# Kernel tuning notes

Measured on AMD Instinct MI355X. Metric: run time of the kernel, lower is better.

Reference implementation:

```python
import jax, jax.numpy as jnp
import numpy as np
from jax import lax

BN_EPS = 1e-5
BNS = 1.0 / np.sqrt(1.0 + BN_EPS)  # eval-mode BatchNorm with mean=0, var=1, gamma=1, beta=0


def setup_inputs() -> dict:
    key = jax.random.key(0)
    ks = jax.random.split(key, 12)
    B, Cin, H, W = 8, 256, 128, 128
    NC, HD, RC, NL = 12, 64, 128, 3
    f = lambda k, shp, s: jax.random.normal(k, shp, jnp.float32) * s
    return dict(
        features=f(ks[0], (B, Cin, H, W), 1.0),
        segmentation=jax.random.uniform(ks[1], (B, NC, H, W), dtype=jnp.float32),
        W_rpn=f(ks[2], (RC, Cin, 3, 3), 0.02), b_rpn=jnp.zeros((RC,), jnp.float32),
        W_node=f(ks[3], (HD, RC), 0.08), b_node=jnp.zeros((HD,), jnp.float32),
        W_e1=f(ks[4], (2 * HD, HD), 0.08), b_e1=jnp.zeros((HD,), jnp.float32),
        W_e2=f(ks[5], (HD, HD), 0.1), b_e2=jnp.zeros((HD,), jnp.float32),
        W_g=f(ks[6], (NL, HD, HD), 0.1), b_g=jnp.zeros((NL, HD), jnp.float32),
        ln_g=jnp.ones((NL, HD), jnp.float32), ln_b=jnp.zeros((NL, HD), jnp.float32),
        glob_emb=f(ks[7], (NC, HD), 0.02),
        W_sp=f(ks[8], (HD, RC), 0.1), b_sp=jnp.zeros((RC,), jnp.float32),
    )


def _forward(features, segmentation, W_rpn, b_rpn, W_node, b_node, W_e1, b_e1,
             W_e2, b_e2, W_g, b_g, ln_g, ln_b, glob_emb, W_sp, b_sp):
    B, NC, H, W = segmentation.shape
    HD = W_node.shape[0]
    NL = W_g.shape[0]

    # ---- RegionProposalNetwork: 3x3 conv + BN(eval) + ReLU ----
    refined = lax.conv_general_dilated(
        features, W_rpn, (1, 1), 'SAME',
        dimension_numbers=('NCHW', 'OIHW', 'NCHW'))
    refined = jax.nn.relu((refined + b_rpn[None, :, None, None]) * BNS)  # [B,RC,H,W]

    # per-class 3x3 maxpool on segmentation, threshold -> binary masks
    pooled = lax.reduce_window(segmentation, -jnp.inf, lax.max,
                               (1, 1, 3, 3), (1, 1, 1, 1), 'SAME')
    masks = (pooled > 0.5).astype(features.dtype)  # [B,NC,H,W]

    # ---- NodeFeatureExtractor (1x1 conv is linear: conv(f*m)=(Wf)*m + b) ----
    yw = jnp.einsum('dk,bkhw->bdhw', W_node, refined)            # [B,HD,H,W]
    z = jax.nn.relu((yw + b_node[None, :, None, None]) * BNS)    # value inside mask region
    masked_sum = jnp.einsum('bdhw,bchw->bcd', z, masks)          # [B,NC,HD]
    mask_sum = masks.sum((2, 3))                                 # [B,NC]
    node_feats = masked_sum / (mask_sum[..., None] + 1e-6)       # [B,NC,HD]

    # ---- EdgeFeatureExtractor: all (i,j), i!=j, gated by class presence ----
    pairs = np.array([(i, j) for i in range(NC) for j in range(NC) if i != j])
    src = jnp.asarray(pairs[:, 0])  # [E]
    dst = jnp.asarray(pairs[:, 1])
    present = (mask_sum > 0).astype(features.dtype)              # [B,NC]
    valid = present[:, src] * present[:, dst]                    # [B,E]
    cat = jnp.concatenate([node_feats[:, src], node_feats[:, dst]], axis=-1)  # [B,E,2HD]
    h = jax.nn.relu(cat @ W_e1 + b_e1)
    edge_attr = (h @ W_e2 + b_e2) * valid[..., None]             # [B,E,HD]

    # ---- TissueGraphNetwork ----
    presence = (node_feats.sum(-1) != 0).astype(features.dtype)[..., None]  # [B,NC,1]
    seg_sum = jax.vmap(lambda m: jax.ops.segment_sum(m, dst, num_segments=NC))
    x = node_feats
    for l in range(NL):
        xw = x @ W_g[l]                                          # [B,NC,HD]
        msgs = xw[:, src] * edge_attr                            # [B,E,HD]
        agg = seg_sum(msgs) + b_g[l]
        xr = jax.nn.relu(agg)
        mu = xr.mean(-1, keepdims=True)
        var = ((xr - mu) ** 2).mean(-1, keepdims=True)
        normed = (xr - mu) / jnp.sqrt(var + 1e-5) * ln_g[l] + ln_b[l]
        x = normed + x if l > 0 else normed
    x = x * presence + glob_emb[None] * (1.0 - presence)         # [B,NC,HD]

    # ---- SpatialProjector ----
    spatial = jnp.einsum('bcd,bchw->bdhw', x, masks)             # [B,HD,H,W]
    out = jnp.einsum('do,bdhw->bohw', W_sp, spatial)             # [B,RC,H,W]
    out = jax.nn.relu((out + b_sp[None, :, None, None]) * BNS)
    return out


def reference(features, segmentation, W_rpn, b_rpn, W_node, b_node, W_e1, b_e1,
              W_e2, b_e2, W_g, b_g, ln_g, ln_b, glob_emb, W_sp, b_sp):
    return _forward(features, segmentation, W_rpn, b_rpn, W_node, b_node,
                    W_e1, b_e1, W_e2, b_e2, W_g, b_g, ln_g, ln_b,
                    glob_emb, W_sp, b_sp)
```

## Files before the change

### kernel.cpp

```cpp
#include <hip/hip_runtime.h>
#include <math.h>

#define BNS_F 0.9999950000374998f

typedef short short8 __attribute__((ext_vector_type(8)));
typedef float f32x4 __attribute__((ext_vector_type(4)));
typedef __attribute__((address_space(3))) void lds_void;
typedef const __attribute__((address_space(1))) void glb_void;

__device__ __forceinline__ unsigned short f2bf(float f) {
    unsigned u = __builtin_bit_cast(unsigned, f);
    unsigned r = (u + 0x7fffu + ((u >> 16) & 1u)) >> 16;
    return (unsigned short)r;
}
__device__ __forceinline__ float bf2f(unsigned short h) {
    unsigned u = ((unsigned)h) << 16;
    return __builtin_bit_cast(float, u);
}

__global__ __launch_bounds__(256) void convert_feat(
    const float* __restrict__ feat, unsigned short* __restrict__ Fbt)
{
    __shared__ unsigned short sb[64 * 270];
    int b = blockIdx.x >> 8;
    int px0 = (blockIdx.x & 255) * 64;
    int t = threadIdx.x, l = t & 63, w = t >> 6;

    for (int r = 0; r < 64; ++r) {
        int ic = r * 4 + w;
        float v = feat[((size_t)(b * 256 + ic)) * 16384 + px0 + l];
        sb[l * 270 + ic] = f2bf(v);
    }
    __syncthreads();

    uint4* dst = (uint4*)(Fbt + ((size_t)(b * 16384 + px0)) * 256);
    #pragma unroll
    for (int k = 0; k < 8; ++k) {
        int idx = k * 256 + t;
        int px = idx >> 5, piece = idx & 31;
        dst[idx] = *(const uint4*)(sb + px * 270 + piece * 8);
    }
}

__global__ __launch_bounds__(256) void reorg_w(
    const float* __restrict__ Wrpn, unsigned short* __restrict__ Wr)
{
    int oc = blockIdx.x;
    int ic = threadIdx.x;
    const float* src = Wrpn + ((size_t)oc * 256 + ic) * 9;
    #pragma unroll
    for (int tap = 0; tap < 9; ++tap)
        Wr[((size_t)tap * 128 + oc) * 256 + ic] = f2bf(src[tap]);
}

__global__ __launch_bounds__(128) void masks_kernel(
    const float* __restrict__ seg, float* __restrict__ masks,
    float* __restrict__ mask_sum)
{
    int bid = blockIdx.x;
    int h = bid & 127;
    int c = (bid >> 7) % 12;
    int b = bid / (128 * 12);
    int px = threadIdx.x;

    const float* s = seg + ((size_t)(b * 12 + c) * 128) * 128;
    float m = -INFINITY;
    #pragma unroll
    for (int dy = -1; dy <= 1; ++dy) {
        int y = h + dy;
        if (y < 0 || y > 127) continue;
        #pragma unroll
        for (int dx = -1; dx <= 1; ++dx) {
            int x = px + dx;
            if (x < 0 || x > 127) continue;
            m = fmaxf(m, s[y * 128 + x]);
        }
    }
    float v = (m > 0.5f) ? 1.0f : 0.0f;
    masks[((size_t)(b * 12 + c) * 128 + h) * 128 + px] = v;

    float cnt = v;
    #pragma unroll
    for (int off = 1; off < 64; off <<= 1) cnt += __shfl_xor(cnt, off, 64);
    if ((threadIdx.x & 63) == 0) atomicAdd(&mask_sum[b * 12 + c], cnt);
}

#define SWZ(col) (((col) >> 1) & 3)
#define BUF_BYTES 24960

__global__ __launch_bounds__(512) void conv_node_kernel(
    const unsigned short* __restrict__ Fbt, const unsigned short* __restrict__ Wr,
    const float* __restrict__ brpn, const float* __restrict__ Wnode,
    const float* __restrict__ bnode, const float* __restrict__ masks,
    const float* __restrict__ zero16, float* __restrict__ ms_rep)
{
    __shared__ __align__(16) unsigned char lds[49920];

    int wg = blockIdx.x;
    int bid = (wg & 7) * 128 + (wg >> 3);
    int h = bid & 127, b = bid >> 7;

    int t = threadIdx.x;
    int lane = t & 63;
    int wv = __builtin_amdgcn_readfirstlane(t >> 6);
    int mg = wv >> 1;
    int ng = wv & 1;
    int kg = lane >> 4;
    int ln15 = lane & 15;

    f32x4 acc[2][4];
    #pragma unroll
    for (int i = 0; i < 2; ++i)
        #pragma unroll
        for (int j = 0; j < 4; ++j) acc[i][j] = (f32x4){0.f, 0.f, 0.f, 0.f};

    const size_t fb_base = (size_t)b * 16384 * 256;

    auto stage = [&](int bsel, int ic0) {
        for (int c0 = 0; c0 < 1560; c0 += 512) {
            int c = c0 + t;
            unsigned ldsoff = (unsigned)bsel * BUF_BYTES + (unsigned)(c0 + wv * 64) * 16;
            if (c < 1560) {
                int sp = c & 3, cr = c >> 2;
                int col = cr % 130, row = cr / 130;
                int sl = (sp - SWZ(col)) & 3;
                int y = h - 1 + row;
                int x = col - 1;
                const void* gsrc = ((unsigned)y < 128u && (unsigned)x < 128u)
                    ? (const void*)(Fbt + fb_base + (size_t)(y * 128 + x) * 256
                                    + ic0 + sl * 8)
                    : (const void*)zero16;
                __builtin_amdgcn_global_load_lds(
                    (glb_void*)gsrc, (lds_void*)(lds + ldsoff), 16, 0, 0);
            }
        }
    };

    stage(0, 0);
    __syncthreads();

    for (int s = 0; s < 8; ++s) {
        int ic0 = s * 32;
        const unsigned char* buf = lds + (s & 1) * BUF_BYTES;

        #pragma unroll
        for (int dy = 0; dy < 3; ++dy) {
            #pragma unroll
            for (int dxi = 0; dxi < 3; ++dxi) {
                int tap = dy * 3 + dxi;
                const unsigned short* wp =
                    Wr + ((size_t)(tap * 128 + mg * 32 + ln15) * 256 + ic0 + kg * 8);
                short8 a0 = *(const short8*)wp;
                short8 a1 = *(const short8*)(wp + (size_t)16 * 256);
                short8 bf[4];
                #pragma unroll
                for (int nt = 0; nt < 4; ++nt) {
                    int col = ng * 64 + nt * 16 + ln15 + dxi;
                    unsigned off =
                        (unsigned)((dy * 130 + col) * 4 + ((kg + SWZ(col)) & 3)) * 16;
                    bf[nt] = *(const short8*)(buf + off);
                }
                #pragma unroll
                for (int nt = 0; nt < 4; ++nt) {
                    acc[0][nt] = __builtin_amdgcn_mfma_f32_16x16x32_bf16(
                        a0, bf[nt], acc[0][nt], 0, 0, 0);
                    acc[1][nt] = __builtin_amdgcn_mfma_f32_16x16x32_bf16(
                        a1, bf[nt], acc[1][nt], 0, 0, 0);
                }
            }
        }

        if (s < 7) stage((s + 1) & 1, ic0 + 32);
        __syncthreads();
    }

    unsigned short* refined = (unsigned short*)lds;
    #pragma unroll
    for (int mt = 0; mt < 2; ++mt) {
        #pragma unroll
        for (int nt = 0; nt < 4; ++nt) {
            int px = ng * 64 + nt * 16 + ln15;
            #pragma unroll
            for (int r = 0; r < 4; ++r) {
                int oc = mg * 32 + mt * 16 + kg * 4 + r;
                float v = fmaxf((acc[mt][nt][r] + brpn[oc]) * BNS_F, 0.f);
                refined[oc * 130 + px] = f2bf(v);
            }
        }
    }
    __syncthreads();

    float z0[8], z1[8];
    #pragma unroll
    for (int j = 0; j < 8; ++j) { z0[j] = 0.f; z1[j] = 0.f; }
    const float* wn = Wnode + (size_t)wv * 8 * 128;
    for (int k = 0; k < 128; ++k) {
        float r0 = bf2f(refined[k * 130 + lane]);
        float r1 = bf2f(refined[k * 130 + 64 + lane]);
        #pragma unroll
        for (int j = 0; j < 8; ++j) {
            float w = wn[j * 128 + k];
            z0[j] = fmaf(w, r0, z0[j]);
            z1[j] = fmaf(w, r1, z1[j]);
        }
    }
    #pragma unroll
    for (int j = 0; j < 8; ++j) {
        float bb = bnode[wv * 8 + j];
        z0[j] = fmaxf((z0[j] + bb) * BNS_F, 0.f);
        z1[j] = fmaxf((z1[j] + bb) * BNS_F, 0.f);
    }

    int rep = bid & 7;
    const float* mrow = masks + ((size_t)b * 12 * 128 + h) * 128;
    float* msb = ms_rep + ((size_t)(rep * 8 + b) * 12) * 64 + wv * 8;
    for (int c = 0; c < 12; ++c) {
        float m0 = mrow[(size_t)c * 16384 + lane];
        float m1 = mrow[(size_t)c * 16384 + 64 + lane];
        #pragma unroll
        for (int j = 0; j < 8; ++j) {
            float v = fmaf(z0[j], m0, z1[j] * m1);
            #pragma unroll
            for (int off2 = 1; off2 < 64; off2 <<= 1) v += __shfl_xor(v, off2, 64);
            if (lane == 0) atomicAdd(&msb[c * 64 + j], v);
        }
    }
}

__global__ __launch_bounds__(256) void edge_kernel(
    const float* __restrict__ ms_rep, const float* __restrict__ mask_sum,
    const float* __restrict__ We1, const float* __restrict__ be1,
    const float* __restrict__ We2, const float* __restrict__ be2,
    float* __restrict__ ea_g)
{
    int gb = blockIdx.x;
    int b = gb / 33, eg = gb % 33;
    int wv = threadIdx.x >> 6, d = threadIdx.x & 63;
    int e = eg * 4 + wv;
    int src = e / 11, jj = e % 11;
    int dst = jj + (jj >= src ? 1 : 0);

    float mssrc = 0.f, msdst = 0.f;
    #pragma unroll
    for (int rep = 0; rep < 8; ++rep) {
        mssrc += ms_rep[((size_t)(rep * 8 + b) * 12 + src) * 64 + d];
        msdst += ms_rep[((size_t)(rep * 8 + b) * 12 + dst) * 64 + d];
    }
    float cs = mask_sum[b * 12 + src], cd = mask_sum[b * 12 + dst];
    float nsrc = mssrc / (cs + 1e-6f);
    float ndst = msdst / (cd + 1e-6f);

    float hv = be1[d];
    for (int k = 0; k < 64; ++k) hv = fmaf(__shfl(nsrc, k, 64), We1[k * 64 + d], hv);
    for (int k = 0; k < 64; ++k) hv = fmaf(__shfl(ndst, k, 64), We1[(64 + k) * 64 + d], hv);
    hv = fmaxf(hv, 0.f);
    float av = be2[d];
    for (int k = 0; k < 64; ++k) av = fmaf(__shfl(hv, k, 64), We2[k * 64 + d], av);

    float valid = ((cs > 0.f) ? 1.f : 0.f) * ((cd > 0.f) ? 1.f : 0.f);
    ea_g[((size_t)b * 132 + e) * 64 + d] = av * valid;
}

__global__ __launch_bounds__(256) void graph_kernel(
    const float* __restrict__ ms_rep, const float* __restrict__ mask_sum,
    const float* __restrict__ ea_g,
    const float* __restrict__ Wg, const float* __restrict__ bg,
    const float* __restrict__ lng, const float* __restrict__ lnb,
    const float* __restrict__ glob, const float* __restrict__ Wsp,
    float* __restrict__ xs_out)
{
    __shared__ float nf[12 * 64];
    __shared__ float x [12 * 64];
    __shared__ float xw[12 * 64];
    __shared__ float ea[132 * 64];
    __shared__ float presence[12];

    int b = blockIdx.x;
    int t = threadIdx.x;

    for (int i = t; i < 768; i += 256) {
        int c = i >> 6, d = i & 63;
        float ms = 0.f;
        #pragma unroll
        for (int rep = 0; rep < 8; ++rep)
            ms += ms_rep[((size_t)(rep * 8 + b) * 12 + c) * 64 + d];
        nf[i] = ms / (mask_sum[b * 12 + c] + 1e-6f);
    }
    for (int i = t; i < 132 * 64; i += 256) ea[i] = ea_g[(size_t)b * 8448 + i];
    __syncthreads();

    for (int i = t; i < 768; i += 256) {
        int c = i >> 6;
        float v = nf[i];
        #pragma unroll
        for (int off = 1; off < 64; off <<= 1) v += __shfl_xor(v, off, 64);
        if ((i & 63) == 0) presence[c] = (v != 0.f) ? 1.f : 0.f;
        x[i] = nf[i];
    }
    __syncthreads();

    for (int l = 0; l < 3; ++l) {
        const float* wg = Wg + l * 4096;
        for (int i = t; i < 768; i += 256) {
            int c = i >> 6, d = i & 63;
            float v = 0.f;
            for (int k = 0; k < 64; ++k) v = fmaf(x[c * 64 + k], wg[k * 64 + d], v);
            xw[i] = v;
        }
        __syncthreads();
        for (int i = t; i < 768; i += 256) {
            int j = i >> 6, d = i & 63;
            float agg = bg[l * 64 + d];
            #pragma unroll
            for (int src2 = 0; src2 < 12; ++src2) {
                if (src2 == j) continue;
                int jj2 = j - (j > src2 ? 1 : 0);
                int e = src2 * 11 + jj2;
                agg = fmaf(xw[src2 * 64 + d], ea[e * 64 + d], agg);
            }
            float xr = fmaxf(agg, 0.f);
            float s = xr;
            #pragma unroll
            for (int off = 1; off < 64; off <<= 1) s += __shfl_xor(s, off, 64);
            float mu = s * (1.f / 64.f);
            float df = xr - mu;
            float s2 = df * df;
            #pragma unroll
            for (int off = 1; off < 64; off <<= 1) s2 += __shfl_xor(s2, off, 64);
            float var = s2 * (1.f / 64.f);
            float normed = df * (1.0f / sqrtf(var + 1e-5f)) * lng[l * 64 + d]
                           + lnb[l * 64 + d];
            nf[i] = (l > 0) ? (normed + x[i]) : normed;
        }
        __syncthreads();
        for (int i = t; i < 768; i += 256) x[i] = nf[i];
        __syncthreads();
    }

    for (int i = t; i < 768; i += 256) {
        int c = i >> 6;
        float p = presence[c];
        x[i] = x[i] * p + glob[c * 64 + (i & 63)] * (1.f - p);
    }
    __syncthreads();

    for (int i = t; i < 12 * 128; i += 256) {
        int c = i >> 7, o = i & 127;
        float v = 0.f;
        for (int k = 0; k < 64; ++k) v = fmaf(x[c * 64 + k], Wsp[k * 128 + o], v);
        xs_out[b * 1536 + i] = v;
    }
}

__global__ __launch_bounds__(256) void out_kernel(
    const float* __restrict__ xs, const float* __restrict__ masks,
    const float* __restrict__ bsp, float* __restrict__ out)
{
    __shared__ float xsl[12 * 128];
    __shared__ float ml[12 * 128];
    int bid = blockIdx.x;
    int h = bid & 127;
    int b = bid >> 7;
    int t = threadIdx.x;

    for (int i = t; i < 1536; i += 256) xsl[i] = xs[b * 1536 + i];
    for (int i = t; i < 1536; i += 256) {
        int c = i >> 7, px = i & 127;
        ml[i] = masks[((size_t)(b * 12 + c) * 128 + h) * 128 + px];
    }
    __syncthreads();

    int px = t & 127;
    int og = t >> 7;
    float m[12];
    #pragma unroll
    for (int c = 0; c < 12; ++c) m[c] = ml[c * 128 + px];

    float* ob = out + ((size_t)b * 128 * 128 + h) * 128 + px;
    for (int i = 0; i < 64; ++i) {
        int o = og * 64 + i;
        float s = 0.f;
        #pragma unroll
        for (int c = 0; c < 12; ++c) s = fmaf(xsl[c * 128 + o], m[c], s);
        ob[(size_t)o * 16384] = fmaxf((s + bsp[o]) * BNS_F, 0.f);
    }
}

extern "C" void kernel_launch(void* const* d_in, const int* in_sizes, int n_in,
                              void* d_out, int out_size, void* d_ws, size_t ws_size,
                              hipStream_t stream)
{
    const float* feat  = (const float*)d_in[0];
    const float* seg   = (const float*)d_in[1];
    const float* Wrpn  = (const float*)d_in[2];
    const float* brpn  = (const float*)d_in[3];
    const float* Wnode = (const float*)d_in[4];
    const float* bnode = (const float*)d_in[5];
    const float* We1   = (const float*)d_in[6];
    const float* be1   = (const float*)d_in[7];
    const float* We2   = (const float*)d_in[8];
    const float* be2   = (const float*)d_in[9];
    const float* Wg    = (const float*)d_in[10];
    const float* bg    = (const float*)d_in[11];
    const float* lng   = (const float*)d_in[12];
    const float* lnb   = (const float*)d_in[13];
    const float* glob  = (const float*)d_in[14];
    const float* Wsp   = (const float*)d_in[15];
    const float* bsp   = (const float*)d_in[16];
    float* out = (float*)d_out;

    unsigned short* Fbt = (unsigned short*)d_out;

    float* masks    = (float*)d_ws;
    float* ms_rep   = masks + 1572864;
    float* mask_sum = ms_rep + 49152;
    float* zero16   = mask_sum + 96;
    float* xs       = zero16 + 8;
    float* ea_g     = xs + 12288;
    unsigned short* Wr = (unsigned short*)(ea_g + 67584);

    hipMemsetAsync(ms_rep, 0, (49152 + 96 + 8) * sizeof(float), stream);

    convert_feat<<<2048, 256, 0, stream>>>(feat, Fbt);
    reorg_w<<<128, 256, 0, stream>>>(Wrpn, Wr);
    masks_kernel<<<8 * 12 * 128, 128, 0, stream>>>(seg, masks, mask_sum);
    conv_node_kernel<<<1024, 512, 0, stream>>>(Fbt, Wr, brpn, Wnode, bnode,
                                               masks, zero16, ms_rep);
    edge_kernel<<<264, 256, 0, stream>>>(ms_rep, mask_sum, We1, be1, We2, be2, ea_g);
    graph_kernel<<<8, 256, 0, stream>>>(ms_rep, mask_sum, ea_g,
                                        Wg, bg, lng, lnb, glob, Wsp, xs);
    out_kernel<<<1024, 256, 0, stream>>>(xs, masks, bsp, out);
}
```

Measured before the change: 455.9 us.

## Chunk-major bf16 feature layout with register-staged single-buffer conv loads

Changes the converted feature layout from pixel-major with 256 channels to chunks of 8 channels laid out over all pixels. This lets convert_feat run without an LDS transpose, using coalesced per-chunk stores. The conv kernel drops the async global_load_lds double buffer and instead prefetches the next channel slice into registers while computing, then writes it to a single LDS buffer after a barrier. LDS use shrinks, which may raise occupancy, at the cost of an extra barrier per stage and more register pressure. The new layout also spreads each pixel's channels across strided chunks, which may hurt the locality of the gathers.

New measurement: 465.8 us. 1.02x slower.

```diff
diff --git a/kernel.cpp b/kernel.cpp
--- a/kernel.cpp
+++ b/kernel.cpp
@@ -5,8 +5,6 @@
 
 typedef short short8 __attribute__((ext_vector_type(8)));
 typedef float f32x4 __attribute__((ext_vector_type(4)));
-typedef __attribute__((address_space(3))) void lds_void;
-typedef const __attribute__((address_space(1))) void glb_void;
 
 __device__ __forceinline__ unsigned short f2bf(float f) {
     unsigned u = __builtin_bit_cast(unsigned, f);
@@ -21,25 +19,22 @@
 __global__ __launch_bounds__(256) void convert_feat(
     const float* __restrict__ feat, unsigned short* __restrict__ Fbt)
 {
-    __shared__ unsigned short sb[64 * 270];
-    int b = blockIdx.x >> 8;
-    int px0 = (blockIdx.x & 255) * 64;
-    int t = threadIdx.x, l = t & 63, w = t >> 6;
-
-    for (int r = 0; r < 64; ++r) {
-        int ic = r * 4 + w;
-        float v = feat[((size_t)(b * 256 + ic)) * 16384 + px0 + l];
-        sb[l * 270 + ic] = f2bf(v);
-    }
-    __syncthreads();
-
-    uint4* dst = (uint4*)(Fbt + ((size_t)(b * 16384 + px0)) * 256);
-    #pragma unroll
-    for (int k = 0; k < 8; ++k) {
-        int idx = k * 256 + t;
-        int px = idx >> 5, piece = idx & 31;
-        dst[idx] = *(const uint4*)(sb + px * 270 + piece * 8);
-    }
+    int bid = blockIdx.x;
+    int pxc = bid & 63;
+    int icg = (bid >> 6) & 31;
+    int b   = bid >> 11;
+    int px  = pxc * 256 + threadIdx.x;
+
+    const float* src = feat + ((size_t)(b * 256 + icg * 8)) * 16384 + px;
+    unsigned v[4];
+    #pragma unroll
+    for (int i = 0; i < 4; ++i) {
+        unsigned lo = f2bf(src[(size_t)(2 * i)     * 16384]);
+        unsigned hi = f2bf(src[(size_t)(2 * i + 1) * 16384]);
+        v[i] = lo | (hi << 16);
+    }
+    uint4 o; o.x = v[0]; o.y = v[1]; o.z = v[2]; o.w = v[3];
+    *(uint4*)(Fbt + (((size_t)(b * 32 + icg) * 16384) + px) * 8) = o;
 }
 
 __global__ __launch_bounds__(256) void reorg_w(
@@ -86,7 +81,7 @@
 }
 
 #define SWZ(col) (((col) >> 1) & 3)
-#define BUF_BYTES 24960
+#define CHUNK_STRIDE (4 * 16384 * 8)
 
 __global__ __launch_bounds__(512) void conv_node_kernel(
     const unsigned short* __restrict__ Fbt, const unsigned short* __restrict__ Wr,
@@ -94,7 +89,7 @@
     const float* __restrict__ bnode, const float* __restrict__ masks,
     const float* __restrict__ zero16, float* __restrict__ ms_rep)
 {
-    __shared__ __align__(16) unsigned char lds[49920];
+    __shared__ __align__(16) unsigned char lds[33280];
 
     int wg = blockIdx.x;
     int bid = (wg & 7) * 128 + (wg >> 3);
@@ -114,34 +109,51 @@
         #pragma unroll
         for (int j = 0; j < 4; ++j) acc[i][j] = (f32x4){0.f, 0.f, 0.f, 0.f};
 
-    const size_t fb_base = (size_t)b * 16384 * 256;
-
-    auto stage = [&](int bsel, int ic0) {
-        for (int c0 = 0; c0 < 1560; c0 += 512) {
-            int c = c0 + t;
-            unsigned ldsoff = (unsigned)bsel * BUF_BYTES + (unsigned)(c0 + wv * 64) * 16;
-            if (c < 1560) {
-                int sp = c & 3, cr = c >> 2;
-                int col = cr % 130, row = cr / 130;
-                int sl = (sp - SWZ(col)) & 3;
-                int y = h - 1 + row;
-                int x = col - 1;
-                const void* gsrc = ((unsigned)y < 128u && (unsigned)x < 128u)
-                    ? (const void*)(Fbt + fb_base + (size_t)(y * 128 + x) * 256
-                                    + ic0 + sl * 8)
-                    : (const void*)zero16;
-                __builtin_amdgcn_global_load_lds(
-                    (glb_void*)gsrc, (lds_void*)(lds + ldsoff), 16, 0, 0);
-            }
-        }
-    };
-
-    stage(0, 0);
+    const unsigned short* p[4];
+    size_t inc[4];
+    unsigned woff[4];
+    bool act3 = (t < 24);
+    #pragma unroll
+    for (int r = 0; r < 4; ++r) {
+        int c = (r < 3) ? (r * 512 + t) : (1536 + t);
+        bool act = (r < 3) || act3;
+        int sp = c & 3, cr = c >> 2;
+        int col = cr % 130, row = cr / 130;
+        int sl = (sp - SWZ(col)) & 3;
+        int y = h - 1 + row;
+        int x = col - 1;
+        bool in = ((unsigned)y < 128u) && ((unsigned)x < 128u) && act;
+        p[r]   = in ? (Fbt + (((size_t)(b * 32 + sl) * 16384) + y * 128 + x) * 8)
+                    : (const unsigned short*)zero16;
+        inc[r] = in ? (size_t)CHUNK_STRIDE : 0;
+        woff[r] = (unsigned)c * 16;
+    }
+
+    {
+        uint4 s0 = *(const uint4*)p[0];
+        uint4 s1 = *(const uint4*)p[1];
+        uint4 s2 = *(const uint4*)p[2];
+        uint4 s3 = act3 ? *(const uint4*)p[3] : (uint4){0, 0, 0, 0};
+        p[0] += inc[0]; p[1] += inc[1]; p[2] += inc[2]; p[3] += inc[3];
+        *(uint4*)(lds + woff[0]) = s0;
+        *(uint4*)(lds + woff[1]) = s1;
+        *(uint4*)(lds + woff[2]) = s2;
+        if (act3) *(uint4*)(lds + woff[3]) = s3;
+    }
     __syncthreads();
 
     for (int s = 0; s < 8; ++s) {
         int ic0 = s * 32;
-        const unsigned char* buf = lds + (s & 1) * BUF_BYTES;
+
+        uint4 st0, st1, st2, st3;
+        bool pre = (s < 7);
+        if (pre) {
+            st0 = *(const uint4*)p[0];
+            st1 = *(const uint4*)p[1];
+            st2 = *(const uint4*)p[2];
+            st3 = act3 ? *(const uint4*)p[3] : (uint4){0, 0, 0, 0};
+            p[0] += inc[0]; p[1] += inc[1]; p[2] += inc[2]; p[3] += inc[3];
+        }
 
         #pragma unroll
         for (int dy = 0; dy < 3; ++dy) {
@@ -158,7 +170,7 @@
                     int col = ng * 64 + nt * 16 + ln15 + dxi;
                     unsigned off =
                         (unsigned)((dy * 130 + col) * 4 + ((kg + SWZ(col)) & 3)) * 16;
-                    bf[nt] = *(const short8*)(buf + off);
+                    bf[nt] = *(const short8*)(lds + off);
                 }
                 #pragma unroll
                 for (int nt = 0; nt < 4; ++nt) {
@@ -170,8 +182,14 @@
             }
         }
 
-        if (s < 7) stage((s + 1) & 1, ic0 + 32);
         __syncthreads();
+        if (pre) {
+            *(uint4*)(lds + woff[0]) = st0;
+            *(uint4*)(lds + woff[1]) = st1;
+            *(uint4*)(lds + woff[2]) = st2;
+            if (act3) *(uint4*)(lds + woff[3]) = st3;
+            __syncthreads();
+        }
     }
 
     unsigned short* refined = (unsigned short*)lds;
@@ -421,7 +439,7 @@
 
     hipMemsetAsync(ms_rep, 0, (49152 + 96 + 8) * sizeof(float), stream);
 
-    convert_feat<<<2048, 256, 0, stream>>>(feat, Fbt);
+    convert_feat<<<16384, 256, 0, stream>>>(feat, Fbt);
     reorg_w<<<128, 256, 0, stream>>>(Wrpn, Wr);
     masks_kernel<<<8 * 12 * 128, 128, 0, stream>>>(seg, masks, mask_sum);
     conv_node_kernel<<<1024, 512, 0, stream>>>(Fbt, Wr, brpn, Wnode, bnode,
```

## Chunk bf16 feature layout by 8 channels and fuse prep kernels

Applied to the files above, without the earlier changes.

Changes the bf16 feature buffer from pixel-major with 256 channels to chunks of 8 channels per pixel ([B,32,HW,8]). This lets the conversion kernel write without an LDS transpose and lets the conv staging use precomputed pointers that advance by a fixed stride. The feature conversion, weight reorganisation and mask kernels are merged into one launch. The conv kernel also gets a launch_bounds occupancy hint and interleaves its B-fragment loads with the MFMAs. Global reads during staging become more scattered across channel chunks, and the occupancy hint may constrain register allocation.

Result: slower. 492.5 us (+8.0%).

```diff
diff --git a/kernel.cpp b/kernel.cpp
--- a/kernel.cpp
+++ b/kernel.cpp
@@ -18,77 +18,71 @@
     return __builtin_bit_cast(float, u);
 }
 
-__global__ __launch_bounds__(256) void convert_feat(
-    const float* __restrict__ feat, unsigned short* __restrict__ Fbt)
-{
-    __shared__ unsigned short sb[64 * 270];
-    int b = blockIdx.x >> 8;
-    int px0 = (blockIdx.x & 255) * 64;
-    int t = threadIdx.x, l = t & 63, w = t >> 6;
-
-    for (int r = 0; r < 64; ++r) {
-        int ic = r * 4 + w;
-        float v = feat[((size_t)(b * 256 + ic)) * 16384 + px0 + l];
-        sb[l * 270 + ic] = f2bf(v);
-    }
-    __syncthreads();
-
-    uint4* dst = (uint4*)(Fbt + ((size_t)(b * 16384 + px0)) * 256);
-    #pragma unroll
-    for (int k = 0; k < 8; ++k) {
-        int idx = k * 256 + t;
-        int px = idx >> 5, piece = idx & 31;
-        dst[idx] = *(const uint4*)(sb + px * 270 + piece * 8);
-    }
-}
-
-__global__ __launch_bounds__(256) void reorg_w(
-    const float* __restrict__ Wrpn, unsigned short* __restrict__ Wr)
-{
-    int oc = blockIdx.x;
-    int ic = threadIdx.x;
-    const float* src = Wrpn + ((size_t)oc * 256 + ic) * 9;
-    #pragma unroll
-    for (int tap = 0; tap < 9; ++tap)
-        Wr[((size_t)tap * 128 + oc) * 256 + ic] = f2bf(src[tap]);
-}
-
-__global__ __launch_bounds__(128) void masks_kernel(
+__global__ __launch_bounds__(256) void prep_kernel(
+    const float* __restrict__ feat, unsigned short* __restrict__ Fbt,
+    const float* __restrict__ Wrpn, unsigned short* __restrict__ Wr,
     const float* __restrict__ seg, float* __restrict__ masks,
     float* __restrict__ mask_sum)
 {
     int bid = blockIdx.x;
-    int h = bid & 127;
-    int c = (bid >> 7) % 12;
-    int b = bid / (128 * 12);
-    int px = threadIdx.x;
-
-    const float* s = seg + ((size_t)(b * 12 + c) * 128) * 128;
-    float m = -INFINITY;
-    #pragma unroll
-    for (int dy = -1; dy <= 1; ++dy) {
-        int y = h + dy;
-        if (y < 0 || y > 127) continue;
-        #pragma unroll
-        for (int dx = -1; dx <= 1; ++dx) {
-            int x = px + dx;
-            if (x < 0 || x > 127) continue;
-            m = fmaxf(m, s[y * 128 + x]);
-        }
-    }
-    float v = (m > 0.5f) ? 1.0f : 0.0f;
-    masks[((size_t)(b * 12 + c) * 128 + h) * 128 + px] = v;
-
-    float cnt = v;
-    #pragma unroll
-    for (int off = 1; off < 64; off <<= 1) cnt += __shfl_xor(cnt, off, 64);
-    if ((threadIdx.x & 63) == 0) atomicAdd(&mask_sum[b * 12 + c], cnt);
+    int t = threadIdx.x;
+
+    if (bid < 16384) {
+        int pxc = bid & 63;
+        int icg = (bid >> 6) & 31;
+        int b   = bid >> 11;
+        int px  = pxc * 256 + t;
+        const float* src = feat + ((size_t)(b * 256 + icg * 8)) * 16384 + px;
+        unsigned v[4];
+        #pragma unroll
+        for (int i = 0; i < 4; ++i) {
+            unsigned lo = f2bf(src[(size_t)(2 * i)     * 16384]);
+            unsigned hi = f2bf(src[(size_t)(2 * i + 1) * 16384]);
+            v[i] = lo | (hi << 16);
+        }
+        uint4 o; o.x = v[0]; o.y = v[1]; o.z = v[2]; o.w = v[3];
+        *(uint4*)(Fbt + (((size_t)(b * 32 + icg) * 16384) + px) * 8) = o;
+    } else if (bid < 16512) {
+        int oc = bid - 16384;
+        const float* src = Wrpn + ((size_t)oc * 256 + t) * 9;
+        #pragma unroll
+        for (int tap = 0; tap < 9; ++tap)
+            Wr[((size_t)tap * 128 + oc) * 256 + t] = f2bf(src[tap]);
+    } else {
+        int mb = bid - 16512;
+        int h = (mb & 63) * 2 + (t >> 7);
+        int c = (mb >> 6) % 12;
+        int b = mb / (64 * 12);
+        int px = t & 127;
+
+        const float* s = seg + ((size_t)(b * 12 + c) * 128) * 128;
+        float m = -INFINITY;
+        #pragma unroll
+        for (int dy = -1; dy <= 1; ++dy) {
+            int y = h + dy;
+            if (y < 0 || y > 127) continue;
+            #pragma unroll
+            for (int dx = -1; dx <= 1; ++dx) {
+                int x = px + dx;
+                if (x < 0 || x > 127) continue;
+                m = fmaxf(m, s[y * 128 + x]);
+            }
+        }
+        float v = (m > 0.5f) ? 1.0f : 0.0f;
+        masks[((size_t)(b * 12 + c) * 128 + h) * 128 + px] = v;
+
+        float cnt = v;
+        #pragma unroll
+        for (int off = 1; off < 64; off <<= 1) cnt += __shfl_xor(cnt, off, 64);
+        if ((t & 63) == 0) atomicAdd(&mask_sum[b * 12 + c], cnt);
+    }
 }
 
 #define SWZ(col) (((col) >> 1) & 3)
 #define BUF_BYTES 24960
-
-__global__ __launch_bounds__(512) void conv_node_kernel(
+#define CHUNK_ELEMS (4u * 16384u * 8u)
+
+__global__ __launch_bounds__(512, 6) void conv_node_kernel(
     const unsigned short* __restrict__ Fbt, const unsigned short* __restrict__ Wr,
     const float* __restrict__ brpn, const float* __restrict__ Wnode,
     const float* __restrict__ bnode, const float* __restrict__ masks,
@@ -114,29 +108,40 @@
         #pragma unroll
         for (int j = 0; j < 4; ++j) acc[i][j] = (f32x4){0.f, 0.f, 0.f, 0.f};
 
-    const size_t fb_base = (size_t)b * 16384 * 256;
-
-    auto stage = [&](int bsel, int ic0) {
-        for (int c0 = 0; c0 < 1560; c0 += 512) {
-            int c = c0 + t;
-            unsigned ldsoff = (unsigned)bsel * BUF_BYTES + (unsigned)(c0 + wv * 64) * 16;
-            if (c < 1560) {
-                int sp = c & 3, cr = c >> 2;
-                int col = cr % 130, row = cr / 130;
-                int sl = (sp - SWZ(col)) & 3;
-                int y = h - 1 + row;
-                int x = col - 1;
-                const void* gsrc = ((unsigned)y < 128u && (unsigned)x < 128u)
-                    ? (const void*)(Fbt + fb_base + (size_t)(y * 128 + x) * 256
-                                    + ic0 + sl * 8)
-                    : (const void*)zero16;
-                __builtin_amdgcn_global_load_lds(
-                    (glb_void*)gsrc, (lds_void*)(lds + ldsoff), 16, 0, 0);
-            }
-        }
+    const unsigned short* zp = (const unsigned short*)zero16;
+
+    const unsigned short* pp[4];
+    #pragma unroll
+    for (int r = 0; r < 4; ++r) {
+        int c = (r < 3) ? (r * 512 + t) : (1536 + t);
+        bool act = (r < 3) || (t < 24);
+        int sp = c & 3, cr = c >> 2;
+        int col = cr % 130, row = cr / 130;
+        int sl = (sp - SWZ(col)) & 3;
+        int y = h - 1 + row, x = col - 1;
+        bool in = act && ((unsigned)y < 128u) && ((unsigned)x < 128u);
+        pp[r] = in ? (Fbt + (((size_t)(b * 32 + sl) * 16384) + y * 128 + x) * 8)
+                   : zp;
+    }
+
+    auto stage = [&](int bsel) {
+        #pragma unroll
+        for (int r = 0; r < 3; ++r) {
+            unsigned ldsoff = (unsigned)bsel * BUF_BYTES
+                            + (unsigned)(r * 512 + wv * 64) * 16;
+            __builtin_amdgcn_global_load_lds((glb_void*)pp[r],
+                (lds_void*)(lds + ldsoff), 16, 0, 0);
+            pp[r] += (pp[r] == zp) ? 0u : CHUNK_ELEMS;
+        }
+        if (t < 24) {
+            unsigned ldsoff = (unsigned)bsel * BUF_BYTES + 1536u * 16;
+            __builtin_amdgcn_global_load_lds((glb_void*)pp[3],
+                (lds_void*)(lds + ldsoff), 16, 0, 0);
+        }
+        pp[3] += (pp[3] == zp) ? 0u : CHUNK_ELEMS;
     };
 
-    stage(0, 0);
+    stage(0);
     __syncthreads();
 
     for (int s = 0; s < 8; ++s) {
@@ -152,25 +157,32 @@
                     Wr + ((size_t)(tap * 128 + mg * 32 + ln15) * 256 + ic0 + kg * 8);
                 short8 a0 = *(const short8*)wp;
                 short8 a1 = *(const short8*)(wp + (size_t)16 * 256);
-                short8 bf[4];
                 #pragma unroll
-                for (int nt = 0; nt < 4; ++nt) {
-                    int col = ng * 64 + nt * 16 + ln15 + dxi;
-                    unsigned off =
-                        (unsigned)((dy * 130 + col) * 4 + ((kg + SWZ(col)) & 3)) * 16;
-                    bf[nt] = *(const short8*)(buf + off);
-                }
-                #pragma unroll
-                for (int nt = 0; nt < 4; ++nt) {
-                    acc[0][nt] = __builtin_amdgcn_mfma_f32_16x16x32_bf16(
-                        a0, bf[nt], acc[0][nt], 0, 0, 0);
-                    acc[1][nt] = __builtin_amdgcn_mfma_f32_16x16x32_bf16(
-                        a1, bf[nt], acc[1][nt], 0, 0, 0);
+                for (int np = 0; np < 2; ++np) {
+                    short8 b0, b1;
+                    {
+                        int col0 = ng * 64 + (np * 2) * 16 + ln15 + dxi;
+                        unsigned off0 = (unsigned)((dy * 130 + col0) * 4
+                                        + ((kg + SWZ(col0)) & 3)) * 16;
+                        b0 = *(const short8*)(buf + off0);
+                        int col1 = col0 + 16;
+                        unsigned off1 = (unsigned)((dy * 130 + col1) * 4
+                                        + ((kg + SWZ(col1)) & 3)) * 16;
+                        b1 = *(const short8*)(buf + off1);
+                    }
+                    acc[0][np * 2]     = __builtin_amdgcn_mfma_f32_16x16x32_bf16(
+                        a0, b0, acc[0][np * 2], 0, 0, 0);
+                    acc[1][np * 2]     = __builtin_amdgcn_mfma_f32_16x16x32_bf16(
+                        a1, b0, acc[1][np * 2], 0, 0, 0);
+                    acc[0][np * 2 + 1] = __builtin_amdgcn_mfma_f32_16x16x32_bf16(
+                        a0, b1, acc[0][np * 2 + 1], 0, 0, 0);
+                    acc[1][np * 2 + 1] = __builtin_amdgcn_mfma_f32_16x16x32_bf16(
+                        a1, b1, acc[1][np * 2 + 1], 0, 0, 0);
                 }
             }
         }
 
-        if (s < 7) stage((s + 1) & 1, ic0 + 32);
+        if (s < 7) stage((s + 1) & 1);
         __syncthreads();
     }
 
@@ -421,9 +433,7 @@
 
     hipMemsetAsync(ms_rep, 0, (49152 + 96 + 8) * sizeof(float), stream);
 
-    convert_feat<<<2048, 256, 0, stream>>>(feat, Fbt);
-    reorg_w<<<128, 256, 0, stream>>>(Wrpn, Wr);
-    masks_kernel<<<8 * 12 * 128, 128, 0, stream>>>(seg, masks, mask_sum);
+    prep_kernel<<<22656, 256, 0, stream>>>(feat, Fbt, Wrpn, Wr, seg, masks, mask_sum);
     conv_node_kernel<<<1024, 512, 0, stream>>>(Fbt, Wr, brpn, Wnode, bnode,
                                                masks, zero16, ms_rep);
     edge_kernel<<<264, 256, 0, stream>>>(ms_rep, mask_sum, We1, be1, We2, be2, ea_g);
```
